# Optimization experiments

Measured on AMD Instinct MI355X. Metric: run time of the kernel, lower is better.

## Reference

```python
import jax, jax.numpy as jnp
import numpy as np

B, T, D, H = 4, 2048, 1024, 16
DH = D // H


def setup_inputs() -> dict:
    key = jax.random.key(0)
    ks = jax.random.split(key, 5)
    x = jax.random.normal(ks[0], (B, T, D), dtype=jnp.float32)
    W_qkv = jax.random.normal(ks[1], (D, 3 * D), dtype=jnp.float32) * 0.02
    b_qkv = jax.random.normal(ks[2], (3 * D,), dtype=jnp.float32) * 0.02
    W_o = jax.random.normal(ks[3], (D, D), dtype=jnp.float32) * 0.02
    b_o = jax.random.normal(ks[4], (D,), dtype=jnp.float32) * 0.02
    return {"x": x, "W_qkv": W_qkv, "b_qkv": b_qkv, "W_o": W_o, "b_o": b_o}


def reference(x, W_qkv, b_qkv, W_o, b_o):
    b, t, d = x.shape
    qkv = x @ W_qkv + b_qkv                      # [b, t, 3*d]
    # 'b t (k h dh) -> k b h t dh'
    qkv = qkv.reshape(b, t, 3, H, DH).transpose(2, 0, 3, 1, 4)
    q, k, v = qkv[0], qkv[1], qkv[2]             # each [b, h, t, dh]
    scores = jnp.einsum('bhqd,bhkd->bhqk', q, k) / jnp.sqrt(jnp.float32(DH))
    causal_mask = jnp.triu(jnp.ones((t, t), dtype=bool), k=1)  # True above diag
    scores = jnp.where(causal_mask, -jnp.inf, scores)
    attn = jax.nn.softmax(scores, axis=-1)       # [b, h, t, t]
    o = jnp.einsum('bhqk,bhkd->bqhd', attn, v).reshape(b, t, d)
    return o @ W_o + b_o
```

## Files before the change

### kernel.cpp

```cpp
#include <hip/hip_runtime.h>
#include <hip/hip_bf16.h>

typedef __attribute__((ext_vector_type(8))) short bh8;
typedef __attribute__((ext_vector_type(4))) float f32x4;

#define GBL(p) (const __attribute__((address_space(1))) void*)(p)
#define LDSP(p) (__attribute__((address_space(3))) void*)(p)

__device__ __forceinline__ ushort f2bf(float f){
  union { float f; unsigned u; } v; v.f = f;
  unsigned u = v.u;
  return (ushort)((u + 0x7fffu + ((u >> 16) & 1u)) >> 16);
}

__global__ __launch_bounds__(256) void cast_x_kernel(const float4* __restrict__ in,
                                                     ushort* __restrict__ out){
  int i = blockIdx.x * 256 + threadIdx.x;
  float4 v = in[i];
  ushort4 o;
  o.x = f2bf(v.x); o.y = f2bf(v.y); o.z = f2bf(v.z); o.w = f2bf(v.w);
  *(ushort4*)&out[(size_t)i * 4] = o;
}

__global__ __launch_bounds__(256) void transpose_cast_kernel(const float* __restrict__ in,
                                                             ushort* __restrict__ out,
                                                             int R, int C){
  __shared__ float tile[32][33];
  int bx = blockIdx.x * 32;
  int by = blockIdx.y * 32;
  int tx = threadIdx.x, ty = threadIdx.y;
  #pragma unroll
  for (int i = 0; i < 32; i += 8)
    tile[ty + i][tx] = in[(size_t)(by + ty + i) * C + bx + tx];
  __syncthreads();
  #pragma unroll
  for (int i = 0; i < 32; i += 8)
    out[(size_t)(bx + ty + i) * R + by + tx] = f2bf(tile[tx][ty + i]);
}

__global__ __launch_bounds__(256) void gemm_qkv_kernel(
    const ushort* __restrict__ A,
    const ushort* __restrict__ Bt,
    const float* __restrict__ bias,
    ushort* __restrict__ Qd, ushort* __restrict__ Kd, ushort* __restrict__ Vt)
{
  constexpr int K = 1024;
  __shared__ ushort sA[8192];
  __shared__ ushort sB[8192];
  const int tid = threadIdx.x;
  const int lane = tid & 63, wave = tid >> 6;
  const int quad = lane >> 4, l16 = lane & 15;
  const int rx7 = l16 & 7;
  const int wm = (wave >> 1) * 64, wn = (wave & 1) * 64;
  const size_t aBase = (size_t)blockIdx.x * 128 * K;
  const size_t bBase = (size_t)blockIdx.y * 128 * K;
  f32x4 acc[4][4] = {};
  for (int k0 = 0; k0 < K; k0 += 64){
    #pragma unroll
    for (int c = 0; c < 4; c++){
      int u = c * 256 + tid;
      int row = u >> 3, cu = (u & 7) ^ (row & 7);
      __builtin_amdgcn_global_load_lds(GBL(A + aBase + (size_t)row * K + k0 + cu * 8),
                                       LDSP(&sA[u * 8]), 16, 0, 0);
      __builtin_amdgcn_global_load_lds(GBL(Bt + bBase + (size_t)row * K + k0 + cu * 8),
                                       LDSP(&sB[u * 8]), 16, 0, 0);
    }
    __syncthreads();
    #pragma unroll
    for (int ks = 0; ks < 2; ks++){
      bh8 af[4], bf[4];
      #pragma unroll
      for (int i = 0; i < 4; i++){
        int row = wm + i * 16 + l16;
        af[i] = *(const bh8*)&sA[row * 64 + (((ks * 4 + quad) ^ rx7) << 3)];
      }
      #pragma unroll
      for (int j = 0; j < 4; j++){
        int row = wn + j * 16 + l16;
        bf[j] = *(const bh8*)&sB[row * 64 + (((ks * 4 + quad) ^ rx7) << 3)];
      }
      #pragma unroll
      for (int i = 0; i < 4; i++)
        #pragma unroll
        for (int j = 0; j < 4; j++)
          acc[i][j] = __builtin_amdgcn_mfma_f32_16x16x32_bf16(af[i], bf[j], acc[i][j], 0, 0, 0);
    }
    __syncthreads();
  }
  const int whichBlk = (blockIdx.y * 128) >> 10;
  #pragma unroll
  for (int i = 0; i < 4; i++){
    int mg = blockIdx.x * 128 + wm + i * 16 + quad * 4;
    int bb = mg >> 11, t0 = mg & 2047;
    #pragma unroll
    for (int j = 0; j < 4; j++){
      int ng = blockIdx.y * 128 + wn + j * 16 + l16;
      float bv = bias[ng];
      int h = (ng >> 6) & 15;
      int dh = ng & 63;
      if (whichBlk == 2){
        ushort4 o;
        o.x = f2bf(acc[i][j][0] + bv);
        o.y = f2bf(acc[i][j][1] + bv);
        o.z = f2bf(acc[i][j][2] + bv);
        o.w = f2bf(acc[i][j][3] + bv);
        *(ushort4*)&Vt[((size_t)((bb * 16 + h) * 64 + dh)) * 2048 + t0] = o;
      } else {
        ushort* dst = (whichBlk == 0) ? Qd : Kd;
        float sc = (whichBlk == 0) ? 0.18033688f : 1.0f;
        #pragma unroll
        for (int r = 0; r < 4; r++)
          dst[((size_t)((bb * 16 + h) * 2048 + t0 + r) << 6) + dh] = f2bf((acc[i][j][r] + bv) * sc);
      }
    }
  }
}

__global__ __launch_bounds__(256, 4) void flash_attn_kernel(
    const ushort* __restrict__ Qd, const ushort* __restrict__ Kd,
    const ushort* __restrict__ Vt, ushort* __restrict__ Od)
{
  __shared__ ushort sK[2][4096];
  __shared__ ushort sV[2][4096];
  __shared__ ushort sP[4][1024];
  const int tid = threadIdx.x;
  const int lane = tid & 63, wave = tid >> 6;
  const int quad = lane >> 4, l16 = lane & 15;
  const int bh = blockIdx.x, pairI = blockIdx.y;
  const size_t base = (size_t)bh * (2048 * 64);
  const float SINIT = -7.2134752f;

  const int p0 = tid, p1 = 256 + tid;
  const int r0 = p0 >> 3, c0 = (p0 & 7) ^ (r0 & 7);
  const int r1 = p1 >> 3, c1 = (p1 & 7) ^ (r1 & 7);
  const ushort* kp0 = Kd + base + r0 * 64 + c0 * 8;
  const ushort* kp1 = Kd + base + r1 * 64 + c1 * 8;
  const ushort* vp0 = Vt + base + (size_t)r0 * 2048 + c0 * 8;
  const ushort* vp1 = Vt + base + (size_t)r1 * 2048 + c1 * 8;

  const int b = bh >> 4, h = bh & 15;

  #pragma unroll 1
  for (int phase = 0; phase < 2; phase++){
    const int qt = phase ? pairI : (31 - pairI);
    const ushort* qrow = Qd + base + (size_t)(qt * 64 + wave * 16 + l16) * 64 + quad * 8;
    bh8 qf0 = *(const bh8*)qrow;
    bh8 qf1 = *(const bh8*)(qrow + 32);

    f32x4 Oacc[4] = {};
    float lpart[4] = {0.f, 0.f, 0.f, 0.f};

    __syncthreads();
    __builtin_amdgcn_global_load_lds(GBL(kp0), LDSP(&sK[0][p0 * 8]), 16, 0, 0);
    __builtin_amdgcn_global_load_lds(GBL(kp1), LDSP(&sK[0][p1 * 8]), 16, 0, 0);
    __builtin_amdgcn_global_load_lds(GBL(vp0), LDSP(&sV[0][p0 * 8]), 16, 0, 0);
    __builtin_amdgcn_global_load_lds(GBL(vp1), LDSP(&sV[0][p1 * 8]), 16, 0, 0);

    #pragma unroll 1
    for (int kt = 0; kt <= qt; kt++){
      const int buf = kt & 1;
      __syncthreads();
      if (kt < qt){
        const int nb = buf ^ 1;
        __builtin_amdgcn_global_load_lds(GBL(kp0 + (kt + 1) * 4096), LDSP(&sK[nb][p0 * 8]), 16, 0, 0);
        __builtin_amdgcn_global_load_lds(GBL(kp1 + (kt + 1) * 4096), LDSP(&sK[nb][p1 * 8]), 16, 0, 0);
        __builtin_amdgcn_global_load_lds(GBL(vp0 + (kt + 1) * 64),   LDSP(&sV[nb][p0 * 8]), 16, 0, 0);
        __builtin_amdgcn_global_load_lds(GBL(vp1 + (kt + 1) * 64),   LDSP(&sV[nb][p1 * 8]), 16, 0, 0);
      }
      f32x4 S[4];
      #pragma unroll
      for (int j = 0; j < 4; j++) S[j] = (f32x4){SINIT, SINIT, SINIT, SINIT};
      __builtin_amdgcn_s_setprio(1);
      #pragma unroll
      for (int ks = 0; ks < 2; ks++){
        bh8 aq = ks ? qf1 : qf0;
        #pragma unroll
        for (int j = 0; j < 4; j++){
          int row = j * 16 + l16;
          int u = row * 8 + ((ks * 4 + quad) ^ (row & 7));
          bh8 bk = *(const bh8*)&sK[buf][u * 8];
          S[j] = __builtin_amdgcn_mfma_f32_16x16x32_bf16(aq, bk, S[j], 0, 0, 0);
        }
      }
      __builtin_amdgcn_s_setprio(0);
      if (kt == qt){
        #pragma unroll
        for (int j = 0; j < 4; j++)
          #pragma unroll
          for (int r = 0; r < 4; r++){
            int relq = wave * 16 + quad * 4 + r;
            int relt = j * 16 + l16;
            if (relt > relq) S[j][r] = -1e30f;
          }
      }
      #pragma unroll
      for (int j = 0; j < 4; j++){
        float pv[4];
        #pragma unroll
        for (int r = 0; r < 4; r++){
          pv[r] = exp2f(S[j][r]);
          lpart[r] += pv[r];
        }
        __hip_bfloat162 pk0 = __float22bfloat162_rn({pv[0], pv[1]});
        __hip_bfloat162 pk1 = __float22bfloat162_rn({pv[2], pv[3]});
        ushort2 w0 = *(ushort2*)&pk0, w1 = *(ushort2*)&pk1;
        ushort w[4] = {w0.x, w0.y, w1.x, w1.y};
        #pragma unroll
        for (int r = 0; r < 4; r++){
          int row = quad * 4 + r;
          int cu = 2 * j + (l16 >> 3);
          int phys = row * 8 + (cu ^ (row & 7));
          sP[wave][phys * 8 + (l16 & 7)] = w[r];
        }
      }
      __builtin_amdgcn_s_setprio(1);
      #pragma unroll
      for (int ks = 0; ks < 2; ks++){
        int up = l16 * 8 + ((ks * 4 + quad) ^ (l16 & 7));
        bh8 ap = *(const bh8*)&sP[wave][up * 8];
        #pragma unroll
        for (int j = 0; j < 4; j++){
          int row = j * 16 + l16;
          int u = row * 8 + ((ks * 4 + quad) ^ (row & 7));
          bh8 bv = *(const bh8*)&sV[buf][u * 8];
          Oacc[j] = __builtin_amdgcn_mfma_f32_16x16x32_bf16(ap, bv, Oacc[j], 0, 0, 0);
        }
      }
      __builtin_amdgcn_s_setprio(0);
    }
    float lr[4];
    #pragma unroll
    for (int r = 0; r < 4; r++){
      float s = lpart[r];
      s += __shfl_xor(s, 1, 64);
      s += __shfl_xor(s, 2, 64);
      s += __shfl_xor(s, 4, 64);
      s += __shfl_xor(s, 8, 64);
      lr[r] = 1.0f / s;
    }
    #pragma unroll
    for (int j = 0; j < 4; j++)
      #pragma unroll
      for (int r = 0; r < 4; r++){
        int qg = qt * 64 + wave * 16 + quad * 4 + r;
        int dh = j * 16 + l16;
        Od[(size_t)(b * 2048 + qg) * 1024 + h * 64 + dh] = f2bf(Oacc[j][r] * lr[r]);
      }
  }
}

__global__ __launch_bounds__(256) void gemm_out_kernel(
    const ushort* __restrict__ A,
    const ushort* __restrict__ Bt,
    const float* __restrict__ bias,
    float* __restrict__ out)
{
  constexpr int K = 1024;
  __shared__ ushort sA[8192];
  __shared__ ushort sB[8192];
  const int tid = threadIdx.x;
  const int lane = tid & 63, wave = tid >> 6;
  const int quad = lane >> 4, l16 = lane & 15;
  const int rx7 = l16 & 7;
  const int wm = (wave >> 1) * 64, wn = (wave & 1) * 64;
  const size_t aBase = (size_t)blockIdx.x * 128 * K;
  const size_t bBase = (size_t)blockIdx.y * 128 * K;
  f32x4 acc[4][4] = {};
  for (int k0 = 0; k0 < K; k0 += 64){
    #pragma unroll
    for (int c = 0; c < 4; c++){
      int u = c * 256 + tid;
      int row = u >> 3, cu = (u & 7) ^ (row & 7);
      __builtin_amdgcn_global_load_lds(GBL(A + aBase + (size_t)row * K + k0 + cu * 8),
                                       LDSP(&sA[u * 8]), 16, 0, 0);
      __builtin_amdgcn_global_load_lds(GBL(Bt + bBase + (size_t)row * K + k0 + cu * 8),
                                       LDSP(&sB[u * 8]), 16, 0, 0);
    }
    __syncthreads();
    #pragma unroll
    for (int ks = 0; ks < 2; ks++){
      bh8 af[4], bf[4];
      #pragma unroll
      for (int i = 0; i < 4; i++){
        int row = wm + i * 16 + l16;
        af[i] = *(const bh8*)&sA[row * 64 + (((ks * 4 + quad) ^ rx7) << 3)];
      }
      #pragma unroll
      for (int j = 0; j < 4; j++){
        int row = wn + j * 16 + l16;
        bf[j] = *(const bh8*)&sB[row * 64 + (((ks * 4 + quad) ^ rx7) << 3)];
      }
      #pragma unroll
      for (int i = 0; i < 4; i++)
        #pragma unroll
        for (int j = 0; j < 4; j++)
          acc[i][j] = __builtin_amdgcn_mfma_f32_16x16x32_bf16(af[i], bf[j], acc[i][j], 0, 0, 0);
    }
    __syncthreads();
  }
  #pragma unroll
  for (int i = 0; i < 4; i++){
    int gm = blockIdx.x * 128 + wm + i * 16 + quad * 4;
    #pragma unroll
    for (int j = 0; j < 4; j++){
      int ng = blockIdx.y * 128 + wn + j * 16 + l16;
      float bv = bias[ng];
      #pragma unroll
      for (int r = 0; r < 4; r++)
        out[(size_t)(gm + r) * 1024 + ng] = acc[i][j][r] + bv;
    }
  }
}

extern "C" void kernel_launch(void* const* d_in, const int* in_sizes, int n_in,
                              void* d_out, int out_size, void* d_ws, size_t ws_size,
                              hipStream_t stream) {
  const float* x    = (const float*)d_in[0];
  const float* Wqkv = (const float*)d_in[1];
  const float* bqkv = (const float*)d_in[2];
  const float* Wo   = (const float*)d_in[3];
  const float* bo   = (const float*)d_in[4];
  float* out = (float*)d_out;

  char* p = (char*)d_ws;
  ushort* xb  = (ushort*)p;
  ushort* WqT = (ushort*)(p + 16777216);
  ushort* WoT = (ushort*)(p + 16777216 + 6291456);
  ushort* Qd  = (ushort*)(p + 25165824);
  ushort* Kd  = (ushort*)(p + 25165824 + 16777216);
  ushort* Vt  = (ushort*)(p + 25165824 + 33554432);
  ushort* Od  = xb;

  cast_x_kernel<<<8192, 256, 0, stream>>>((const float4*)x, xb);
  transpose_cast_kernel<<<dim3(96, 32), dim3(32, 8), 0, stream>>>(Wqkv, WqT, 1024, 3072);
  transpose_cast_kernel<<<dim3(32, 32), dim3(32, 8), 0, stream>>>(Wo, WoT, 1024, 1024);
  gemm_qkv_kernel<<<dim3(64, 24), 256, 0, stream>>>(xb, WqT, bqkv, Qd, Kd, Vt);
  flash_attn_kernel<<<dim3(64, 16), 256, 0, stream>>>(Qd, Kd, Vt, Od);
  gemm_out_kernel<<<dim3(64, 8), 256, 0, stream>>>(Od, WoT, bo, out);
}
```

Baseline: 262.1 us.

## Compute transposed S^T tiles and pass P through registers via lane shuffles

Swaps the MFMA operand order so each lane holds a column of scores for one query row. The P tile is then rebuilt in the register layout the PV MFMA needs, using xor-32/16 cross-lane shuffles, instead of being written to and read back from LDS. This removes the sP shared buffer, its scattered 16-bit stores and its reads. It also shortens the row-sum reduction and turns the output stores into vectorised 8-byte writes. The cost is extra permute/shuffle instructions and selects on every tile.

Result: slower. 271.8 us (+3.7%).

```diff
diff --git a/kernel.cpp b/kernel.cpp
--- a/kernel.cpp
+++ b/kernel.cpp
@@ -122,10 +122,10 @@
 {
   __shared__ ushort sK[2][4096];
   __shared__ ushort sV[2][4096];
-  __shared__ ushort sP[4][1024];
   const int tid = threadIdx.x;
   const int lane = tid & 63, wave = tid >> 6;
   const int quad = lane >> 4, l16 = lane & 15;
+  const int b4 = quad & 1, b5 = quad >> 1;
   const int bh = blockIdx.x, pairI = blockIdx.y;
   const size_t base = (size_t)bh * (2048 * 64);
   const float SINIT = -7.2134752f;
@@ -140,6 +140,15 @@
 
   const int b = bh >> 4, h = bh & 15;
 
+  int foff[2][4];
+  #pragma unroll
+  for (int ks = 0; ks < 2; ks++)
+    #pragma unroll
+    for (int j = 0; j < 4; j++){
+      int row = j * 16 + l16;
+      foff[ks][j] = (row * 8 + ((ks * 4 + quad) ^ (row & 7))) * 8;
+    }
+
   #pragma unroll 1
   for (int phase = 0; phase < 2; phase++){
     const int qt = phase ? pairI : (31 - pairI);
@@ -148,7 +157,7 @@
     bh8 qf1 = *(const bh8*)(qrow + 32);
 
     f32x4 Oacc[4] = {};
-    float lpart[4] = {0.f, 0.f, 0.f, 0.f};
+    float lsum = 0.f;
 
     __syncthreads();
     __builtin_amdgcn_global_load_lds(GBL(kp0), LDSP(&sK[0][p0 * 8]), 16, 0, 0);
@@ -176,76 +185,75 @@
         bh8 aq = ks ? qf1 : qf0;
         #pragma unroll
         for (int j = 0; j < 4; j++){
-          int row = j * 16 + l16;
-          int u = row * 8 + ((ks * 4 + quad) ^ (row & 7));
-          bh8 bk = *(const bh8*)&sK[buf][u * 8];
-          S[j] = __builtin_amdgcn_mfma_f32_16x16x32_bf16(aq, bk, S[j], 0, 0, 0);
+          bh8 bk = *(const bh8*)&sK[buf][foff[ks][j]];
+          S[j] = __builtin_amdgcn_mfma_f32_16x16x32_bf16(bk, aq, S[j], 0, 0, 0);
         }
       }
       __builtin_amdgcn_s_setprio(0);
       if (kt == qt){
+        const int relq = wave * 16 + l16;
         #pragma unroll
         for (int j = 0; j < 4; j++)
           #pragma unroll
           for (int r = 0; r < 4; r++){
-            int relq = wave * 16 + quad * 4 + r;
-            int relt = j * 16 + l16;
+            int relt = j * 16 + quad * 4 + r;
             if (relt > relq) S[j][r] = -1e30f;
           }
       }
+      unsigned w[4][2];
       #pragma unroll
       for (int j = 0; j < 4; j++){
         float pv[4];
         #pragma unroll
         for (int r = 0; r < 4; r++){
           pv[r] = exp2f(S[j][r]);
-          lpart[r] += pv[r];
+          lsum += pv[r];
         }
         __hip_bfloat162 pk0 = __float22bfloat162_rn({pv[0], pv[1]});
         __hip_bfloat162 pk1 = __float22bfloat162_rn({pv[2], pv[3]});
-        ushort2 w0 = *(ushort2*)&pk0, w1 = *(ushort2*)&pk1;
-        ushort w[4] = {w0.x, w0.y, w1.x, w1.y};
-        #pragma unroll
-        for (int r = 0; r < 4; r++){
-          int row = quad * 4 + r;
-          int cu = 2 * j + (l16 >> 3);
-          int phys = row * 8 + (cu ^ (row & 7));
-          sP[wave][phys * 8 + (l16 & 7)] = w[r];
+        w[j][0] = *(unsigned*)&pk0;
+        w[j][1] = *(unsigned*)&pk1;
+      }
+      #pragma unroll
+      for (int ks = 0; ks < 2; ks++){
+        unsigned pw[4];
+        #pragma unroll
+        for (int rp = 0; rp < 2; rp++){
+          unsigned t0 = w[2 * ks][rp], t1 = w[2 * ks + 1][rp];
+          unsigned a  = (unsigned)__shfl_xor((int)t0, 32, 64);
+          unsigned bb2= (unsigned)__shfl_xor((int)t1, 32, 64);
+          unsigned R0 = b5 ? bb2 : t0;
+          unsigned R1 = b5 ? t1  : a;
+          unsigned c  = (unsigned)__shfl_xor((int)R0, 16, 64);
+          unsigned d  = (unsigned)__shfl_xor((int)R1, 16, 64);
+          pw[rp]     = b4 ? d  : R0;
+          pw[2 + rp] = b4 ? R1 : c;
         }
-      }
-      __builtin_amdgcn_s_setprio(1);
-      #pragma unroll
-      for (int ks = 0; ks < 2; ks++){
-        int up = l16 * 8 + ((ks * 4 + quad) ^ (l16 & 7));
-        bh8 ap = *(const bh8*)&sP[wave][up * 8];
+        union { unsigned u[4]; bh8 v; } pu;
+        pu.u[0] = pw[0]; pu.u[1] = pw[1]; pu.u[2] = pw[2]; pu.u[3] = pw[3];
+        __builtin_amdgcn_s_setprio(1);
         #pragma unroll
         for (int j = 0; j < 4; j++){
-          int row = j * 16 + l16;
-          int u = row * 8 + ((ks * 4 + quad) ^ (row & 7));
-          bh8 bv = *(const bh8*)&sV[buf][u * 8];
-          Oacc[j] = __builtin_amdgcn_mfma_f32_16x16x32_bf16(ap, bv, Oacc[j], 0, 0, 0);
+          bh8 av = *(const bh8*)&sV[buf][foff[ks][j]];
+          Oacc[j] = __builtin_amdgcn_mfma_f32_16x16x32_bf16(av, pu.v, Oacc[j], 0, 0, 0);
         }
-      }
-      __builtin_amdgcn_s_setprio(0);
-    }
-    float lr[4];
-    #pragma unroll
-    for (int r = 0; r < 4; r++){
-      float s = lpart[r];
-      s += __shfl_xor(s, 1, 64);
-      s += __shfl_xor(s, 2, 64);
-      s += __shfl_xor(s, 4, 64);
-      s += __shfl_xor(s, 8, 64);
-      lr[r] = 1.0f / s;
-    }
-    #pragma unroll
-    for (int j = 0; j < 4; j++)
-      #pragma unroll
-      for (int r = 0; r < 4; r++){
-        int qg = qt * 64 + wave * 16 + quad * 4 + r;
-        int dh = j * 16 + l16;
-        Od[(size_t)(b * 2048 + qg) * 1024 + h * 64 + dh] = f2bf(Oacc[j][r] * lr[r]);
-      }
+        __builtin_amdgcn_s_setprio(0);
+      }
+    }
+    float s = lsum;
+    s += __shfl_xor(s, 16, 64);
+    s += __shfl_xor(s, 32, 64);
+    float lr = 1.0f / s;
+    const int qg = qt * 64 + wave * 16 + l16;
+    #pragma unroll
+    for (int j = 0; j < 4; j++){
+      ushort4 o;
+      o.x = f2bf(Oacc[j][0] * lr);
+      o.y = f2bf(Oacc[j][1] * lr);
+      o.z = f2bf(Oacc[j][2] * lr);
+      o.w = f2bf(Oacc[j][3] * lr);
+      *(ushort4*)&Od[(size_t)(b * 2048 + qg) * 1024 + h * 64 + j * 16 + quad * 4] = o;
+    }
   }
 }
 
```

## Software-pipeline QK^T of next tile with PV via triple-buffered K

Applied to the files above, without the earlier changes.

Triple-buffers K in LDS and prefetches K two tiles ahead. The QK^T MFMAs for tile kt+1 are issued before the PV MFMAs of tile kt, so the softmax exp work and the matrix work of adjacent tiles can overlap. This is meant to hide exp and LDS latency between the two dependent MFMA phases. In exchange, LDS per block grows and the occupancy hint drops from 4 to 3 blocks per CU, with extra registers held for the in-flight S tile.

Result: slower. 269.7 us (+2.9%).

```diff
diff --git a/kernel.cpp b/kernel.cpp
--- a/kernel.cpp
+++ b/kernel.cpp
@@ -116,11 +116,11 @@
   }
 }
 
-__global__ __launch_bounds__(256, 4) void flash_attn_kernel(
+__global__ __launch_bounds__(256, 3) void flash_attn_kernel(
     const ushort* __restrict__ Qd, const ushort* __restrict__ Kd,
     const ushort* __restrict__ Vt, ushort* __restrict__ Od)
 {
-  __shared__ ushort sK[2][4096];
+  __shared__ ushort sK[3][4096];
   __shared__ ushort sV[2][4096];
   __shared__ ushort sP[4][1024];
   const int tid = threadIdx.x;
@@ -155,34 +155,40 @@
     __builtin_amdgcn_global_load_lds(GBL(kp1), LDSP(&sK[0][p1 * 8]), 16, 0, 0);
     __builtin_amdgcn_global_load_lds(GBL(vp0), LDSP(&sV[0][p0 * 8]), 16, 0, 0);
     __builtin_amdgcn_global_load_lds(GBL(vp1), LDSP(&sV[0][p1 * 8]), 16, 0, 0);
-
+    __builtin_amdgcn_global_load_lds(GBL(kp0 + 4096), LDSP(&sK[1][p0 * 8]), 16, 0, 0);
+    __builtin_amdgcn_global_load_lds(GBL(kp1 + 4096), LDSP(&sK[1][p1 * 8]), 16, 0, 0);
+    __syncthreads();
+
+    f32x4 S[4];
+    #pragma unroll
+    for (int j = 0; j < 4; j++) S[j] = (f32x4){SINIT, SINIT, SINIT, SINIT};
+    __builtin_amdgcn_s_setprio(1);
+    #pragma unroll
+    for (int ks = 0; ks < 2; ks++){
+      bh8 aq = ks ? qf1 : qf0;
+      #pragma unroll
+      for (int j = 0; j < 4; j++){
+        int row = j * 16 + l16;
+        int u = row * 8 + ((ks * 4 + quad) ^ (row & 7));
+        bh8 bk = *(const bh8*)&sK[0][u * 8];
+        S[j] = __builtin_amdgcn_mfma_f32_16x16x32_bf16(aq, bk, S[j], 0, 0, 0);
+      }
+    }
+    __builtin_amdgcn_s_setprio(0);
+
+    int slot_next = 1, slot_stage = 2;
     #pragma unroll 1
     for (int kt = 0; kt <= qt; kt++){
-      const int buf = kt & 1;
+      const int vb = kt & 1;
       __syncthreads();
-      if (kt < qt){
-        const int nb = buf ^ 1;
-        __builtin_amdgcn_global_load_lds(GBL(kp0 + (kt + 1) * 4096), LDSP(&sK[nb][p0 * 8]), 16, 0, 0);
-        __builtin_amdgcn_global_load_lds(GBL(kp1 + (kt + 1) * 4096), LDSP(&sK[nb][p1 * 8]), 16, 0, 0);
-        __builtin_amdgcn_global_load_lds(GBL(vp0 + (kt + 1) * 64),   LDSP(&sV[nb][p0 * 8]), 16, 0, 0);
-        __builtin_amdgcn_global_load_lds(GBL(vp1 + (kt + 1) * 64),   LDSP(&sV[nb][p1 * 8]), 16, 0, 0);
-      }
-      f32x4 S[4];
-      #pragma unroll
-      for (int j = 0; j < 4; j++) S[j] = (f32x4){SINIT, SINIT, SINIT, SINIT};
-      __builtin_amdgcn_s_setprio(1);
-      #pragma unroll
-      for (int ks = 0; ks < 2; ks++){
-        bh8 aq = ks ? qf1 : qf0;
-        #pragma unroll
-        for (int j = 0; j < 4; j++){
-          int row = j * 16 + l16;
-          int u = row * 8 + ((ks * 4 + quad) ^ (row & 7));
-          bh8 bk = *(const bh8*)&sK[buf][u * 8];
-          S[j] = __builtin_amdgcn_mfma_f32_16x16x32_bf16(aq, bk, S[j], 0, 0, 0);
-        }
-      }
-      __builtin_amdgcn_s_setprio(0);
+      if (kt + 2 <= qt){
+        __builtin_amdgcn_global_load_lds(GBL(kp0 + (kt + 2) * 4096), LDSP(&sK[slot_stage][p0 * 8]), 16, 0, 0);
+        __builtin_amdgcn_global_load_lds(GBL(kp1 + (kt + 2) * 4096), LDSP(&sK[slot_stage][p1 * 8]), 16, 0, 0);
+      }
+      if (kt + 1 <= qt){
+        __builtin_amdgcn_global_load_lds(GBL(vp0 + (kt + 1) * 64), LDSP(&sV[vb ^ 1][p0 * 8]), 16, 0, 0);
+        __builtin_amdgcn_global_load_lds(GBL(vp1 + (kt + 1) * 64), LDSP(&sV[vb ^ 1][p1 * 8]), 16, 0, 0);
+      }
       if (kt == qt){
         #pragma unroll
         for (int j = 0; j < 4; j++)
@@ -213,6 +219,24 @@
           sP[wave][phys * 8 + (l16 & 7)] = w[r];
         }
       }
+      f32x4 Sn[4];
+      if (kt < qt){
+        #pragma unroll
+        for (int j = 0; j < 4; j++) Sn[j] = (f32x4){SINIT, SINIT, SINIT, SINIT};
+        __builtin_amdgcn_s_setprio(1);
+        #pragma unroll
+        for (int ks = 0; ks < 2; ks++){
+          bh8 aq = ks ? qf1 : qf0;
+          #pragma unroll
+          for (int j = 0; j < 4; j++){
+            int row = j * 16 + l16;
+            int u = row * 8 + ((ks * 4 + quad) ^ (row & 7));
+            bh8 bk = *(const bh8*)&sK[slot_next][u * 8];
+            Sn[j] = __builtin_amdgcn_mfma_f32_16x16x32_bf16(aq, bk, Sn[j], 0, 0, 0);
+          }
+        }
+        __builtin_amdgcn_s_setprio(0);
+      }
       __builtin_amdgcn_s_setprio(1);
       #pragma unroll
       for (int ks = 0; ks < 2; ks++){
@@ -222,11 +246,19 @@
         for (int j = 0; j < 4; j++){
           int row = j * 16 + l16;
           int u = row * 8 + ((ks * 4 + quad) ^ (row & 7));
-          bh8 bv = *(const bh8*)&sV[buf][u * 8];
+          bh8 bv = *(const bh8*)&sV[vb][u * 8];
           Oacc[j] = __builtin_amdgcn_mfma_f32_16x16x32_bf16(ap, bv, Oacc[j], 0, 0, 0);
         }
       }
       __builtin_amdgcn_s_setprio(0);
+      if (kt < qt){
+        #pragma unroll
+        for (int j = 0; j < 4; j++) S[j] = Sn[j];
+      }
+      int t = slot_next;
+      slot_next = slot_stage;
+      slot_stage = (t + 0 == 0) ? 1 : ((slot_stage + 1 == 3) ? 0 : slot_stage + 1);
+      slot_stage = (slot_next + 1 == 3) ? 0 : slot_next + 1;
     }
     float lr[4];
     #pragma unroll
```

## Double-buffer LDS tiles in projection GEMMs with K-step of 32

Applied to the files above, without the earlier changes.

Both projection GEMMs now use two 128x32 LDS buffers per operand and prefetch the next K-slice into the other buffer while the current one feeds the MFMAs. This replaces the single 64-wide buffer with two syncthreads per step. The swizzle is redone for 4 chunks per row, LDS read offsets are precomputed, and s_setprio raises priority around the MFMA block. Launch bounds now request 4 blocks per CU, which may limit registers. The smaller K step doubles the barrier count, and the loop still waits vmcnt(0) every iteration.

Result: no change. 262.6 us (+0.2%).

```diff
diff --git a/kernel.cpp b/kernel.cpp
--- a/kernel.cpp
+++ b/kernel.cpp
@@ -38,55 +38,73 @@
     out[(size_t)(bx + ty + i) * R + by + tx] = f2bf(tile[tx][ty + i]);
 }
 
-__global__ __launch_bounds__(256) void gemm_qkv_kernel(
+__global__ __launch_bounds__(256, 4) void gemm_qkv_kernel(
     const ushort* __restrict__ A,
     const ushort* __restrict__ Bt,
     const float* __restrict__ bias,
     ushort* __restrict__ Qd, ushort* __restrict__ Kd, ushort* __restrict__ Vt)
 {
   constexpr int K = 1024;
-  __shared__ ushort sA[8192];
-  __shared__ ushort sB[8192];
+  __shared__ ushort sA[2][4096];
+  __shared__ ushort sB[2][4096];
   const int tid = threadIdx.x;
   const int lane = tid & 63, wave = tid >> 6;
   const int quad = lane >> 4, l16 = lane & 15;
-  const int rx7 = l16 & 7;
   const int wm = (wave >> 1) * 64, wn = (wave & 1) * 64;
   const size_t aBase = (size_t)blockIdx.x * 128 * K;
   const size_t bBase = (size_t)blockIdx.y * 128 * K;
+
+  const int u0 = tid, u1 = 256 + tid;
+  const int r0 = u0 >> 2, c0 = (u0 & 3) ^ ((r0 ^ (r0 >> 2)) & 3);
+  const int r1 = u1 >> 2, c1 = (u1 & 3) ^ ((r1 ^ (r1 >> 2)) & 3);
+  const ushort* a0 = A + aBase + (size_t)r0 * K + c0 * 8;
+  const ushort* a1 = A + aBase + (size_t)r1 * K + c1 * 8;
+  const ushort* b0 = Bt + bBase + (size_t)r0 * K + c0 * 8;
+  const ushort* b1 = Bt + bBase + (size_t)r1 * K + c1 * 8;
+
+  int aoff[4], boff[4];
+  #pragma unroll
+  for (int i = 0; i < 4; i++){
+    int ra = wm + i * 16 + l16;
+    aoff[i] = (ra * 4 + (quad ^ ((ra ^ (ra >> 2)) & 3))) * 8;
+    int rb = wn + i * 16 + l16;
+    boff[i] = (rb * 4 + (quad ^ ((rb ^ (rb >> 2)) & 3))) * 8;
+  }
+
   f32x4 acc[4][4] = {};
-  for (int k0 = 0; k0 < K; k0 += 64){
-    #pragma unroll
-    for (int c = 0; c < 4; c++){
-      int u = c * 256 + tid;
-      int row = u >> 3, cu = (u & 7) ^ (row & 7);
-      __builtin_amdgcn_global_load_lds(GBL(A + aBase + (size_t)row * K + k0 + cu * 8),
-                                       LDSP(&sA[u * 8]), 16, 0, 0);
-      __builtin_amdgcn_global_load_lds(GBL(Bt + bBase + (size_t)row * K + k0 + cu * 8),
-                                       LDSP(&sB[u * 8]), 16, 0, 0);
-    }
-    __syncthreads();
-    #pragma unroll
-    for (int ks = 0; ks < 2; ks++){
-      bh8 af[4], bf[4];
-      #pragma unroll
-      for (int i = 0; i < 4; i++){
-        int row = wm + i * 16 + l16;
-        af[i] = *(const bh8*)&sA[row * 64 + (((ks * 4 + quad) ^ rx7) << 3)];
-      }
-      #pragma unroll
-      for (int j = 0; j < 4; j++){
-        int row = wn + j * 16 + l16;
-        bf[j] = *(const bh8*)&sB[row * 64 + (((ks * 4 + quad) ^ rx7) << 3)];
-      }
-      #pragma unroll
-      for (int i = 0; i < 4; i++)
-        #pragma unroll
-        for (int j = 0; j < 4; j++)
-          acc[i][j] = __builtin_amdgcn_mfma_f32_16x16x32_bf16(af[i], bf[j], acc[i][j], 0, 0, 0);
-    }
-    __syncthreads();
-  }
+  __builtin_amdgcn_global_load_lds(GBL(a0), LDSP(&sA[0][u0 * 8]), 16, 0, 0);
+  __builtin_amdgcn_global_load_lds(GBL(a1), LDSP(&sA[0][u1 * 8]), 16, 0, 0);
+  __builtin_amdgcn_global_load_lds(GBL(b0), LDSP(&sB[0][u0 * 8]), 16, 0, 0);
+  __builtin_amdgcn_global_load_lds(GBL(b1), LDSP(&sB[0][u1 * 8]), 16, 0, 0);
+  asm volatile("s_waitcnt vmcnt(0)" ::: "memory");
+  __builtin_amdgcn_s_barrier();
+
+  #pragma unroll 2
+  for (int t = 0; t < 32; t++){
+    const int cur = t & 1;
+    if (t < 31){
+      const int nb = cur ^ 1, ko = (t + 1) * 32;
+      __builtin_amdgcn_global_load_lds(GBL(a0 + ko), LDSP(&sA[nb][u0 * 8]), 16, 0, 0);
+      __builtin_amdgcn_global_load_lds(GBL(a1 + ko), LDSP(&sA[nb][u1 * 8]), 16, 0, 0);
+      __builtin_amdgcn_global_load_lds(GBL(b0 + ko), LDSP(&sB[nb][u0 * 8]), 16, 0, 0);
+      __builtin_amdgcn_global_load_lds(GBL(b1 + ko), LDSP(&sB[nb][u1 * 8]), 16, 0, 0);
+    }
+    bh8 af[4], bf[4];
+    #pragma unroll
+    for (int i = 0; i < 4; i++) af[i] = *(const bh8*)&sA[cur][aoff[i]];
+    #pragma unroll
+    for (int j = 0; j < 4; j++) bf[j] = *(const bh8*)&sB[cur][boff[j]];
+    __builtin_amdgcn_s_setprio(1);
+    #pragma unroll
+    for (int i = 0; i < 4; i++)
+      #pragma unroll
+      for (int j = 0; j < 4; j++)
+        acc[i][j] = __builtin_amdgcn_mfma_f32_16x16x32_bf16(af[i], bf[j], acc[i][j], 0, 0, 0);
+    __builtin_amdgcn_s_setprio(0);
+    asm volatile("s_waitcnt vmcnt(0)" ::: "memory");
+    __builtin_amdgcn_s_barrier();
+  }
+
   const int whichBlk = (blockIdx.y * 128) >> 10;
   #pragma unroll
   for (int i = 0; i < 4; i++){
@@ -249,55 +267,73 @@
   }
 }
 
-__global__ __launch_bounds__(256) void gemm_out_kernel(
+__global__ __launch_bounds__(256, 4) void gemm_out_kernel(
     const ushort* __restrict__ A,
     const ushort* __restrict__ Bt,
     const float* __restrict__ bias,
     float* __restrict__ out)
 {
   constexpr int K = 1024;
-  __shared__ ushort sA[8192];
-  __shared__ ushort sB[8192];
+  __shared__ ushort sA[2][4096];
+  __shared__ ushort sB[2][4096];
   const int tid = threadIdx.x;
   const int lane = tid & 63, wave = tid >> 6;
   const int quad = lane >> 4, l16 = lane & 15;
-  const int rx7 = l16 & 7;
   const int wm = (wave >> 1) * 64, wn = (wave & 1) * 64;
   const size_t aBase = (size_t)blockIdx.x * 128 * K;
   const size_t bBase = (size_t)blockIdx.y * 128 * K;
+
+  const int u0 = tid, u1 = 256 + tid;
+  const int r0 = u0 >> 2, c0 = (u0 & 3) ^ ((r0 ^ (r0 >> 2)) & 3);
+  const int r1 = u1 >> 2, c1 = (u1 & 3) ^ ((r1 ^ (r1 >> 2)) & 3);
+  const ushort* a0 = A + aBase + (size_t)r0 * K + c0 * 8;
+  const ushort* a1 = A + aBase + (size_t)r1 * K + c1 * 8;
+  const ushort* b0 = Bt + bBase + (size_t)r0 * K + c0 * 8;
+  const ushort* b1 = Bt + bBase + (size_t)r1 * K + c1 * 8;
+
+  int aoff[4], boff[4];
+  #pragma unroll
+  for (int i = 0; i < 4; i++){
+    int ra = wm + i * 16 + l16;
+    aoff[i] = (ra * 4 + (quad ^ ((ra ^ (ra >> 2)) & 3))) * 8;
+    int rb = wn + i * 16 + l16;
+    boff[i] = (rb * 4 + (quad ^ ((rb ^ (rb >> 2)) & 3))) * 8;
+  }
+
   f32x4 acc[4][4] = {};
-  for (int k0 = 0; k0 < K; k0 += 64){
-    #pragma unroll
-    for (int c = 0; c < 4; c++){
-      int u = c * 256 + tid;
-      int row = u >> 3, cu = (u & 7) ^ (row & 7);
-      __builtin_amdgcn_global_load_lds(GBL(A + aBase + (size_t)row * K + k0 + cu * 8),
-                                       LDSP(&sA[u * 8]), 16, 0, 0);
-      __builtin_amdgcn_global_load_lds(GBL(Bt + bBase + (size_t)row * K + k0 + cu * 8),
-                                       LDSP(&sB[u * 8]), 16, 0, 0);
-    }
-    __syncthreads();
-    #pragma unroll
-    for (int ks = 0; ks < 2; ks++){
-      bh8 af[4], bf[4];
-      #pragma unroll
-      for (int i = 0; i < 4; i++){
-        int row = wm + i * 16 + l16;
-        af[i] = *(const bh8*)&sA[row * 64 + (((ks * 4 + quad) ^ rx7) << 3)];
-      }
-      #pragma unroll
-      for (int j = 0; j < 4; j++){
-        int row = wn + j * 16 + l16;
-        bf[j] = *(const bh8*)&sB[row * 64 + (((ks * 4 + quad) ^ rx7) << 3)];
-      }
-      #pragma unroll
-      for (int i = 0; i < 4; i++)
-        #pragma unroll
-        for (int j = 0; j < 4; j++)
-          acc[i][j] = __builtin_amdgcn_mfma_f32_16x16x32_bf16(af[i], bf[j], acc[i][j], 0, 0, 0);
-    }
-    __syncthreads();
-  }
+  __builtin_amdgcn_global_load_lds(GBL(a0), LDSP(&sA[0][u0 * 8]), 16, 0, 0);
+  __builtin_amdgcn_global_load_lds(GBL(a1), LDSP(&sA[0][u1 * 8]), 16, 0, 0);
+  __builtin_amdgcn_global_load_lds(GBL(b0), LDSP(&sB[0][u0 * 8]), 16, 0, 0);
+  __builtin_amdgcn_global_load_lds(GBL(b1), LDSP(&sB[0][u1 * 8]), 16, 0, 0);
+  asm volatile("s_waitcnt vmcnt(0)" ::: "memory");
+  __builtin_amdgcn_s_barrier();
+
+  #pragma unroll 2
+  for (int t = 0; t < 32; t++){
+    const int cur = t & 1;
+    if (t < 31){
+      const int nb = cur ^ 1, ko = (t + 1) * 32;
+      __builtin_amdgcn_global_load_lds(GBL(a0 + ko), LDSP(&sA[nb][u0 * 8]), 16, 0, 0);
+      __builtin_amdgcn_global_load_lds(GBL(a1 + ko), LDSP(&sA[nb][u1 * 8]), 16, 0, 0);
+      __builtin_amdgcn_global_load_lds(GBL(b0 + ko), LDSP(&sB[nb][u0 * 8]), 16, 0, 0);
+      __builtin_amdgcn_global_load_lds(GBL(b1 + ko), LDSP(&sB[nb][u1 * 8]), 16, 0, 0);
+    }
+    bh8 af[4], bf[4];
+    #pragma unroll
+    for (int i = 0; i < 4; i++) af[i] = *(const bh8*)&sA[cur][aoff[i]];
+    #pragma unroll
+    for (int j = 0; j < 4; j++) bf[j] = *(const bh8*)&sB[cur][boff[j]];
+    __builtin_amdgcn_s_setprio(1);
+    #pragma unroll
+    for (int i = 0; i < 4; i++)
+      #pragma unroll
+      for (int j = 0; j < 4; j++)
+        acc[i][j] = __builtin_amdgcn_mfma_f32_16x16x32_bf16(af[i], bf[j], acc[i][j], 0, 0, 0);
+    __builtin_amdgcn_s_setprio(0);
+    asm volatile("s_waitcnt vmcnt(0)" ::: "memory");
+    __builtin_amdgcn_s_barrier();
+  }
+
   #pragma unroll
   for (int i = 0; i < 4; i++){
     int gm = blockIdx.x * 128 + wm + i * 16 + quad * 4;
```
